# Kernel optimization log

Measured on AMD Instinct MI355X. Metric: run time of the kernel, lower is better.

Reference implementation:

```python
import jax, jax.numpy as jnp
import numpy as np
from jax import lax

MAX_EVENTS = 1024
NHEAD = 8


def _build_events(x, max_events):
    # x: [B, T, C] float in [0,1]. Vectorized run-length encoding.
    B, T, C = x.shape
    xb = (x > 0.5).astype(jnp.int32)
    # run start flags: t=0 is always a start; else value changed vs previous step
    is_start = jnp.concatenate([jnp.ones((B, 1, C), dtype=bool), xb[:, 1:, :] != xb[:, :-1, :]], axis=1)  # [B,T,C]
    t_idx = jnp.arange(T)[None, :, None]  # [1,T,1]
    # next run-start index after t (T if none): suffix-min of start positions
    arr = jnp.where(is_start, t_idx, T)
    suff = lax.cummin(arr, axis=1, reverse=True)
    next_start = jnp.concatenate([suff[:, 1:, :], jnp.full((B, 1, C), T, dtype=suff.dtype)], axis=1)
    duration = next_start - t_idx  # valid at start positions: next change - start
    comp = jnp.arange(C)[None, None, :]
    BIG = jnp.float32(2 * T)
    # sort key identical to torch code: start + component/(C+1); non-starts pushed to the end
    key = jnp.where(is_start, t_idx.astype(jnp.float32) + comp.astype(jnp.float32) / (C + 1.0), BIG)
    keyf = key.reshape(B, T * C)
    order = jnp.argsort(keyf, axis=1)[:, :max_events]  # [B,E] keep earliest events (keys are unique)
    g = lambda a: jnp.take_along_axis(jnp.broadcast_to(a, (B, T, C)).reshape(B, T * C), order, axis=1)
    comp_e = g(comp)
    state_e = g(xb)
    start_e = g(t_idx)
    dur_e = g(duration)
    key_e = jnp.take_along_axis(keyf, order, axis=1)
    mask = (key_e < BIG).astype(x.dtype)  # [B,E]
    onehot = jax.nn.one_hot(comp_e, C, dtype=x.dtype)
    max_start = float(max(1, T - 1))
    rows = jnp.concatenate([
        onehot,
        state_e[..., None].astype(x.dtype),
        start_e[..., None].astype(x.dtype) / max_start,
        dur_e[..., None].astype(x.dtype) / T,
    ], axis=-1)  # [B,E,C+3]
    return rows * mask[..., None], mask


def _ln(z, g, b):
    m = z.mean(-1, keepdims=True)
    v = ((z - m) ** 2).mean(-1, keepdims=True)
    return (z - m) * lax.rsqrt(v + 1e-5) * g + b


def _transformer(h, mask, wq, wk, wv, wo, ln1_g, ln1_b, w1, b1, w2, b2, ln2_g, ln2_b, lnf_g, lnf_b):
    # pre-LN encoder with key-side padding mask; masked mean pooling at the end
    B, E, D = h.shape
    L = wq.shape[0]
    dh = D // NHEAD
    neg = jnp.float32(-1e9)
    kmask = mask[:, None, None, :] > 0  # [B,1,1,E]
    for l in range(L):
        z = _ln(h, ln1_g[l], ln1_b[l])
        q = (z @ wq[l]).reshape(B, E, NHEAD, dh)
        k = (z @ wk[l]).reshape(B, E, NHEAD, dh)
        v = (z @ wv[l]).reshape(B, E, NHEAD, dh)
        s = jnp.einsum('bqhd,bkhd->bhqk', q, k) / jnp.sqrt(jnp.float32(dh))
        s = jnp.where(kmask, s, neg)
        a = jax.nn.softmax(s, axis=-1)
        o = jnp.einsum('bhqk,bkhd->bqhd', a, v).reshape(B, E, D)
        h = h + o @ wo[l]
        z = _ln(h, ln2_g[l], ln2_b[l])
        h = h + (jax.nn.gelu(z @ w1[l] + b1[l]) @ w2[l] + b2[l])
    h = _ln(h, lnf_g, lnf_b)
    denom = jnp.maximum(mask.sum(1, keepdims=True), 1.0)
    return (h * mask[..., None]).sum(1) / denom  # [B,D]


def setup_inputs() -> dict:
    B, T, C = 8, 4096, 8
    D, F, L = 512, 2048, 4
    key = jax.random.key(0)
    ks = jax.random.split(key, 12)
    s = 0.02
    mk = lambda k, shape: jax.random.normal(k, shape, jnp.float32) * s
    return {
        'x': jax.random.uniform(ks[0], (B, T, C), jnp.float32),
        'proj_w': mk(ks[1], (C + 3, D)), 'proj_b': jnp.zeros((D,), jnp.float32),
        'wq': mk(ks[2], (L, D, D)), 'wk': mk(ks[3], (L, D, D)),
        'wv': mk(ks[4], (L, D, D)), 'wo': mk(ks[5], (L, D, D)),
        'ln1_g': jnp.ones((L, D), jnp.float32), 'ln1_b': jnp.zeros((L, D), jnp.float32),
        'w1': mk(ks[6], (L, D, F)), 'b1': jnp.zeros((L, F), jnp.float32),
        'w2': mk(ks[7], (L, F, D)), 'b2': jnp.zeros((L, D), jnp.float32),
        'ln2_g': jnp.ones((L, D), jnp.float32), 'ln2_b': jnp.zeros((L, D), jnp.float32),
        'lnf_g': jnp.ones((D,), jnp.float32), 'lnf_b': jnp.zeros((D,), jnp.float32),
    }


def reference(x, proj_w, proj_b, wq, wk, wv, wo, ln1_g, ln1_b, w1, b1, w2, b2, ln2_g, ln2_b, lnf_g, lnf_b):
    rows, mask = _build_events(x, MAX_EVENTS)
    h = rows @ proj_w + proj_b
    return _transformer(h, mask, wq, wk, wv, wo, ln1_g, ln1_b, w1, b1, w2, b2, ln2_g, ln2_b, lnf_g, lnf_b)
```

## Files before the change

kernel.cpp:

```cpp
#include <hip/hip_runtime.h>
#include <cstdint>
#include <cstddef>


typedef __attribute__((ext_vector_type(8))) short short8;
typedef __attribute__((ext_vector_type(4))) float f32x4;

#define DEVINL __device__ __forceinline__

DEVINL short f2bf(float f) {
  union { float f; unsigned u; } v; v.f = f;
  unsigned u = v.u + 0x7fffu + ((v.u >> 16) & 1u);
  return (short)(u >> 16);
}

DEVINL unsigned bfpack(float lo, float hi) {
  union { float f; unsigned u; } a, b; a.f = lo; b.f = hi;
  return (a.u >> 16) | (b.u & 0xFFFF0000u);
}

DEVINL void gld_lds16(const void* g, void* l) {
  __builtin_amdgcn_global_load_lds(
      (const __attribute__((address_space(1))) void*)g,
      (__attribute__((address_space(3))) void*)l, 16, 0, 0);
}

static constexpr int Bq = 8, T = 4096, C = 8, E = 1024, D = 512, F = 2048;
static constexpr int NL = 4, NH = 8, DH = 64, M = Bq * E;
static constexpr float QSCALE = 0.18033688011112042f;

static constexpr size_t OFF_H    = 0;
static constexpr size_t OFF_Z    = OFF_H    + (size_t)16*1024*1024;
static constexpr size_t OFF_QKV  = OFF_Z    + (size_t)8*1024*1024;
static constexpr size_t OFF_ATT  = OFF_QKV  + (size_t)24*1024*1024;
static constexpr size_t OFF_U    = OFF_ATT  + (size_t)8*1024*1024;
static constexpr size_t OFF_WQKV = OFF_U    + (size_t)32*1024*1024;
static constexpr size_t OFF_WO   = OFF_WQKV + (size_t)6*1024*1024;
static constexpr size_t OFF_W1   = OFF_WO   + (size_t)2*1024*1024;
static constexpr size_t OFF_W2   = OFF_W1   + (size_t)8*1024*1024;
static constexpr size_t OFF_EV   = OFF_W2   + (size_t)8*1024*1024;
static constexpr size_t OFF_NEV  = OFF_EV   + (size_t)131072;
static constexpr size_t OFF_XW   = OFF_NEV  + (size_t)256;

__global__ void tconv_all_kernel(const float* __restrict__ wq, const float* __restrict__ wk,
                                 const float* __restrict__ wv, const float* __restrict__ wo,
                                 const float* __restrict__ w1, const float* __restrict__ w2,
                                 short* __restrict__ wqkv_t, short* __restrict__ wo_t,
                                 short* __restrict__ w1_t, short* __restrict__ w2_t) {
  int bid = blockIdx.x;
  const float* src; short* dst; int N, K, tile;
  if (bid < 4096) {
    int which = bid >> 10, r = bid & 1023, l = r >> 8;
    tile = r & 255; N = 512; K = 512;
    switch (which) {
      case 0:  src = wq + (size_t)l*262144; dst = wqkv_t + (size_t)l*786432;          break;
      case 1:  src = wk + (size_t)l*262144; dst = wqkv_t + (size_t)l*786432 + 262144; break;
      case 2:  src = wv + (size_t)l*262144; dst = wqkv_t + (size_t)l*786432 + 524288; break;
      default: src = wo + (size_t)l*262144; dst = wo_t   + (size_t)l*262144;          break;
    }
  } else if (bid < 8192) {
    int r = bid - 4096, l = r >> 10; tile = r & 1023;
    N = 2048; K = 512;
    src = w1 + (size_t)l*1048576; dst = w1_t + (size_t)l*1048576;
  } else {
    int r = bid - 8192, l = r >> 10; tile = r & 1023;
    N = 512; K = 2048;
    src = w2 + (size_t)l*1048576; dst = w2_t + (size_t)l*1048576;
  }
  int tiles_n = N >> 5;
  int n0 = (tile % tiles_n) * 32, k0 = (tile / tiles_n) * 32;
  __shared__ float tile_s[32][33];
  int tx = threadIdx.x, ty = threadIdx.y;
#pragma unroll
  for (int s = 0; s < 4; ++s)
    tile_s[ty + 8*s][tx] = src[(size_t)(k0 + ty + 8*s) * N + n0 + tx];
  __syncthreads();
#pragma unroll
  for (int s = 0; s < 4; ++s)
    dst[(size_t)(n0 + ty + 8*s) * K + k0 + tx] = f2bf(tile_s[tx][ty + 8*s]);
}

__global__ void xpack_kernel(const float* __restrict__ x, unsigned* __restrict__ xw) {
  __shared__ unsigned char sb[256];
  int idx = blockIdx.x * 256 + threadIdx.x;
  const float* p = x + (size_t)idx * 8;
  f32x4 a = *(const f32x4*)p, b = *(const f32x4*)(p + 4);
  unsigned byte = 0;
#pragma unroll
  for (int j = 0; j < 4; ++j) {
    byte |= (a[j] > 0.5f ? 1u : 0u) << j;
    byte |= (b[j] > 0.5f ? 1u : 0u) << (j + 4);
  }
  sb[threadIdx.x] = (unsigned char)byte;
  __syncthreads();
  if (threadIdx.x < 64)
    xw[blockIdx.x * 64 + threadIdx.x] = *(const unsigned*)(sb + threadIdx.x * 4);
}

__global__ void events_kernel(const unsigned* __restrict__ xw,
                              int4* __restrict__ ev4, int* __restrict__ n_events) {
  int b = blockIdx.x, tid = threadIdx.x;
  int lane = tid & 63, wid = tid >> 6;
  __shared__ int wsum[16];
  const unsigned* xb = xw + b * 1024;
  unsigned word = xb[tid];
  unsigned prevtop = (tid > 0) ? (xb[tid - 1] >> 24) : 0u;
  unsigned flags = word ^ ((word << 8) | prevtop);
  if (tid == 0) flags |= 0xFFu;
  int cnt = __builtin_popcount(flags);

  int v = cnt;
#pragma unroll
  for (int off = 1; off < 64; off <<= 1) {
    int u = __shfl_up(v, off);
    if (lane >= off) v += u;
  }
  if (lane == 63) wsum[wid] = v;
  __syncthreads();
  int base = 0;
  for (int w = 0; w < wid; ++w) base += wsum[w];
  if (tid == 1023) {
    int tot = base + v;
    n_events[b] = tot < E ? tot : E;
  }
  int rank = base + v - cnt;

  unsigned f = flags;
  while (f && rank < E) {
    int bit = __builtin_ctz(f); f &= f - 1;
    int tl = bit >> 3, c = bit & 7;
    int t = tid * 4 + tl;
    int st = (word >> bit) & 1;
    unsigned colm = 0x01010101u << c;
    unsigned above = (bit < 31) ? (flags & colm & (0xFFFFFFFFu << (bit + 1))) : 0u;
    int t2;
    if (above) {
      int nb = __builtin_ctz(above);
      t2 = tid * 4 + ((nb - c) >> 3);
    } else {
      t2 = T;
      for (int w2 = tid + 1; w2 < 1024; ++w2) {
        unsigned nw = xb[w2];
        unsigned fl2 = nw ^ ((nw << 8) | (xb[w2 - 1] >> 24));
        unsigned m2 = fl2 & colm;
        if (m2) { t2 = w2 * 4 + ((__builtin_ctz(m2) - c) >> 3); break; }
      }
    }
    ev4[(b << 10) + rank] = make_int4(c, st, t, t2 - t);
    ++rank;
  }
}

__global__ void embed_kernel(const int4* __restrict__ ev4, const int* __restrict__ nev,
                             const float* __restrict__ pw, const float* __restrict__ pb,
                             float* __restrict__ h) {
  int row = blockIdx.x;
  int b = row >> 10, e = row & 1023;
  int d = threadIdx.x * 4;
  f32x4 acc = *(const f32x4*)(pb + d);
  if (e < nev[b]) {
    int4 e4 = ev4[row];
    float st = (float)e4.y;
    float sn = (float)e4.z * (1.f / 4095.f);
    float dn = (float)e4.w * (1.f / 4096.f);
    acc += *(const f32x4*)(pw + e4.x * D + d);
    acc += st * *(const f32x4*)(pw + 8*D + d);
    acc += sn * *(const f32x4*)(pw + 9*D + d);
    acc += dn * *(const f32x4*)(pw + 10*D + d);
  }
  *(f32x4*)(h + (size_t)row * D + d) = acc;
}

template<int OUTF>
__global__ void ln_kernel(const float* __restrict__ hp, const float* __restrict__ g,
                          const float* __restrict__ bb, void* __restrict__ out) {
  int row = blockIdx.x * 4 + (threadIdx.x >> 6);
  int lane = threadIdx.x & 63;
  int c0 = lane * 8;
  const float* hr = hp + (size_t)row * D;
  f32x4 a = *(const f32x4*)(hr + c0);
  f32x4 c = *(const f32x4*)(hr + c0 + 4);
  float s1 = a[0]+a[1]+a[2]+a[3] + c[0]+c[1]+c[2]+c[3];
  float s2 = a[0]*a[0]+a[1]*a[1]+a[2]*a[2]+a[3]*a[3]
           + c[0]*c[0]+c[1]*c[1]+c[2]*c[2]+c[3]*c[3];
#pragma unroll
  for (int off = 1; off < 64; off <<= 1) {
    s1 += __shfl_xor(s1, off);
    s2 += __shfl_xor(s2, off);
  }
  float mean = s1 * (1.f / 512.f);
  float var  = s2 * (1.f / 512.f) - mean * mean;
  float rstd = rsqrtf(var + 1e-5f);
  f32x4 g0 = *(const f32x4*)(g + c0),  g1 = *(const f32x4*)(g + c0 + 4);
  f32x4 b0 = *(const f32x4*)(bb + c0), b1 = *(const f32x4*)(bb + c0 + 4);
  f32x4 o0 = (a - mean) * rstd * g0 + b0;
  f32x4 o1 = (c - mean) * rstd * g1 + b1;
  if constexpr (OUTF == 0) {
    short8 o;
#pragma unroll
    for (int j = 0; j < 4; ++j) { o[j] = f2bf(o0[j]); o[4 + j] = f2bf(o1[j]); }
    *(short8*)((short*)out + (size_t)row * D + c0) = o;
  } else {
    float* op = (float*)out + (size_t)row * D + c0;
    *(f32x4*)op = o0;
    *(f32x4*)(op + 4) = o1;
  }
}

__global__ void vtrans_kernel(const short* __restrict__ qkv, short* __restrict__ vt) {
  __shared__ short st[64 * 72];
  int et = blockIdx.x, h = blockIdx.y, b = blockIdx.z;
  int tid = threadIdx.x;
  int r8 = tid >> 3, c8 = (tid & 7) * 8;
#pragma unroll
  for (int p = 0; p < 2; ++p) {
    int e = r8 + p * 32;
    short8 v = *(const short8*)(qkv + (size_t)(b*1024 + et*64 + e) * 1536 + 1024 + h*64 + c8);
#pragma unroll
    for (int j = 0; j < 8; ++j) st[(c8 + j) * 72 + e] = v[j];
  }
  __syncthreads();
#pragma unroll
  for (int p = 0; p < 2; ++p) {
    int dd = r8 + p * 32;
    short8 o = *(const short8*)(st + dd * 72 + c8);
    *(short8*)(vt + ((size_t)((b*8 + h) * 64 + dd)) * 1024 + et * 64 + c8) = o;
  }
}

template<int MODE>
__global__ __launch_bounds__(256, 4)
void gemm_kernel(const short* __restrict__ A, const short* __restrict__ Bt,
                 const float* __restrict__ bias, short* __restrict__ O1,
                 int N, int K) {
  __shared__ short a_s[2][128 * 32];
  __shared__ short b_s[2][128 * 32];
  const int tid = threadIdx.x;
  const int wid = tid >> 6, lane = tid & 63;
  const int quad = lane >> 4, l16 = lane & 15;
  const int m0 = blockIdx.y * 128, n0 = blockIdx.x * 128;
  const int wrow = wid >> 1, wcol = wid & 1;
  const int nk = K >> 5;

  const int row0 = tid >> 2, kc0 = tid & 3;
  const int row1 = (tid + 256) >> 2;
  const int ks0 = (kc0 ^ ((row0 >> 1) & 3)) * 8;
  const int ks1 = (kc0 ^ ((row1 >> 1) & 3)) * 8;
  const int ldsoff0 = tid * 8 - lane * 8;
  const int ldsoff1 = (tid + 256) * 8 - lane * 8;

  auto stage = [&](int kt, int buf) {
    int k0 = kt * 32;
    gld_lds16(A  + (size_t)(m0 + row0) * K + k0 + ks0, a_s[buf] + ldsoff0);
    gld_lds16(A  + (size_t)(m0 + row1) * K + k0 + ks1, a_s[buf] + ldsoff1);
    gld_lds16(Bt + (size_t)(n0 + row0) * K + k0 + ks0, b_s[buf] + ldsoff0);
    gld_lds16(Bt + (size_t)(n0 + row1) * K + k0 + ks1, b_s[buf] + ldsoff1);
  };

  f32x4 acc[4][4] = {};

  stage(0, 0);
  asm volatile("s_waitcnt vmcnt(0)" ::: "memory");
  __syncthreads();

  for (int kt = 0; kt < nk; ++kt) {
    const int cur = kt & 1;
    const bool more = (kt + 1) < nk;
    if (more) stage(kt + 1, cur ^ 1);

    short8 af[4], bf[4];
#pragma unroll
    for (int mi = 0; mi < 4; ++mi) {
      int row = wrow*64 + mi*16 + l16;
      int sw = quad ^ ((row >> 1) & 3);
      af[mi] = *(const short8*)(a_s[cur] + row * 32 + sw * 8);
    }
#pragma unroll
    for (int ni = 0; ni < 4; ++ni) {
      int row = wcol*64 + ni*16 + l16;
      int sw = quad ^ ((row >> 1) & 3);
      bf[ni] = *(const short8*)(b_s[cur] + row * 32 + sw * 8);
    }
#pragma unroll
    for (int mi = 0; mi < 4; ++mi)
#pragma unroll
      for (int ni = 0; ni < 4; ++ni)
        acc[mi][ni] = __builtin_amdgcn_mfma_f32_16x16x32_bf16(af[mi], bf[ni], acc[mi][ni], 0, 0, 0);

    if (more) {
      asm volatile("s_waitcnt vmcnt(0)" ::: "memory");
      __syncthreads();
    }
  }

  const int mb = m0 + wrow * 64, nb = n0 + wcol * 64;
#pragma unroll
  for (int mi = 0; mi < 4; ++mi) {
#pragma unroll
    for (int ni = 0; ni < 4; ++ni) {
      int nn = nb + ni * 16 + l16;
#pragma unroll
      for (int r = 0; r < 4; ++r) {
        int mm = mb + mi * 16 + quad * 4 + r;
        float cv = acc[mi][ni][r];
        if constexpr (MODE == 0) {
          float ov = (nn < 512) ? cv * QSCALE : cv;
          union { float f; unsigned u; } vv; vv.f = ov;
          O1[(size_t)mm * N + nn] = (short)(vv.u >> 16);
        } else {
          float xv = cv + bias[nn];
          float x3 = xv * (1.f + 0.044715f * xv * xv);
          float ez = __builtin_amdgcn_exp2f(-2.3022082299f * x3);
          float gv = xv * __builtin_amdgcn_rcpf(1.f + ez);
          union { float f; unsigned u; } vv; vv.f = gv;
          O1[(size_t)mm * N + nn] = (short)(vv.u >> 16);
        }
      }
    }
  }
}

__global__ __launch_bounds__(256, 4)
void gemm64_kernel(const short* __restrict__ A, const short* __restrict__ Bt,
                   const float* __restrict__ bias, float* __restrict__ Cr,
                   int N, int K) {
  __shared__ short a_s[2][64 * 32];
  __shared__ short b_s[2][128 * 32];
  const int tid = threadIdx.x;
  const int wid = tid >> 6, lane = tid & 63;
  const int quad = lane >> 4, l16 = lane & 15;
  const int m0 = blockIdx.y * 64, n0 = blockIdx.x * 128;
  const int nk = K >> 5;

  const int row0 = tid >> 2, kc0 = tid & 3;
  const int row1 = (tid + 256) >> 2;
  const int ksA  = (kc0 ^ (((row0 & 63) >> 1) & 3)) * 8;
  const int ks0  = (kc0 ^ ((row0 >> 1) & 3)) * 8;
  const int ks1  = (kc0 ^ ((row1 >> 1) & 3)) * 8;
  const int ldsoff0 = tid * 8 - lane * 8;
  const int ldsoff1 = (tid + 256) * 8 - lane * 8;

  auto stage = [&](int kt, int buf) {
    int k0 = kt * 32;
    gld_lds16(A  + (size_t)(m0 + row0) * K + k0 + ksA, a_s[buf] + ldsoff0);
    gld_lds16(Bt + (size_t)(n0 + row0) * K + k0 + ks0, b_s[buf] + ldsoff0);
    gld_lds16(Bt + (size_t)(n0 + row1) * K + k0 + ks1, b_s[buf] + ldsoff1);
  };

  f32x4 acc[4][2] = {};

  stage(0, 0);
  asm volatile("s_waitcnt vmcnt(0)" ::: "memory");
  __syncthreads();

  for (int kt = 0; kt < nk; ++kt) {
    const int cur = kt & 1;
    const bool more = (kt + 1) < nk;
    if (more) stage(kt + 1, cur ^ 1);

    short8 af[4], bf[2];
#pragma unroll
    for (int mi = 0; mi < 4; ++mi) {
      int row = mi*16 + l16;
      int sw = quad ^ ((row >> 1) & 3);
      af[mi] = *(const short8*)(a_s[cur] + row * 32 + sw * 8);
    }
#pragma unroll
    for (int ni = 0; ni < 2; ++ni) {
      int row = wid*32 + ni*16 + l16;
      int sw = quad ^ ((row >> 1) & 3);
      bf[ni] = *(const short8*)(b_s[cur] + row * 32 + sw * 8);
    }
#pragma unroll
    for (int mi = 0; mi < 4; ++mi)
#pragma unroll
      for (int ni = 0; ni < 2; ++ni)
        acc[mi][ni] = __builtin_amdgcn_mfma_f32_16x16x32_bf16(af[mi], bf[ni], acc[mi][ni], 0, 0, 0);

    if (more) {
      asm volatile("s_waitcnt vmcnt(0)" ::: "memory");
      __syncthreads();
    }
  }

#pragma unroll
  for (int mi = 0; mi < 4; ++mi) {
#pragma unroll
    for (int ni = 0; ni < 2; ++ni) {
      int nn = n0 + wid*32 + ni * 16 + l16;
#pragma unroll
      for (int r = 0; r < 4; ++r) {
        int mm = m0 + mi * 16 + quad * 4 + r;
        float add = acc[mi][ni][r] + (bias ? bias[nn] : 0.f);
        Cr[(size_t)mm * N + nn] += add;
      }
    }
  }
}

__global__ __launch_bounds__(256, 4)
void attn_kernel(const short* __restrict__ qkv, const short* __restrict__ vt,
                 short* __restrict__ att, const int* __restrict__ n_events) {
  __shared__ short q_s[64 * 64];
  __shared__ short k_s[64 * 64];
  __shared__ short vt_s[64 * 64];
  __shared__ short p_s[64 * 68];
  const int tid = threadIdx.x, wid = tid >> 6, lane = tid & 63;
  const int quad = lane >> 4, l16 = lane & 15;
  const int qt = blockIdx.x, h = blockIdx.y, b = blockIdx.z;
  const int ne = n_events[b];
  const int qbase = b * E + qt * 64;

#pragma unroll
  for (int r = 0; r < 2; ++r) {
    int row = wid * 16 + r * 8 + (lane >> 3);
    int sz = lane & 7, dc = sz ^ (row & 7);
    gld_lds16(qkv + (size_t)(qbase + row) * 1536 + h * 64 + dc * 8,
              q_s + (wid * 16 + r * 8) * 64);
  }
  asm volatile("s_waitcnt vmcnt(0)" ::: "memory");

  short8 qf[2];
#pragma unroll
  for (int ks = 0; ks < 2; ++ks) {
    int row = wid * 16 + l16;
    int dc = (ks * 4 + quad) ^ (row & 7);
    qf[ks] = *(const short8*)(q_s + row * 64 + dc * 8);
  }

  f32x4 accO[4] = {};
  float rs = 0.f;

  for (int kt = 0; kt < 16; ++kt) {
    __syncthreads();
#pragma unroll
    for (int r = 0; r < 2; ++r) {
      int i = (r*4 + wid) * 64 + lane;
      int row = i >> 3, sz = i & 7, dc = sz ^ (row & 7);
      gld_lds16(qkv + (size_t)(b * E + kt * 64 + row) * 1536 + 512 + h * 64 + dc * 8,
                k_s + (r*4 + wid) * 512);
      gld_lds16(vt + (size_t)((b * 8 + h) * 64 + row) * 1024 + kt * 64 + dc * 8,
                vt_s + (r*4 + wid) * 512);
    }
    asm volatile("s_waitcnt vmcnt(0)" ::: "memory");
    __syncthreads();

    f32x4 accS[4] = {};
#pragma unroll
    for (int ni = 0; ni < 4; ++ni) {
#pragma unroll
      for (int ks = 0; ks < 2; ++ks) {
        int row = ni * 16 + l16;
        int dc = (ks * 4 + quad) ^ (row & 7);
        short8 kf = *(const short8*)(k_s + row * 64 + dc * 8);
        accS[ni] = __builtin_amdgcn_mfma_f32_16x16x32_bf16(kf, qf[ks], accS[ni], 0, 0, 0);
      }
    }

    bool full = (kt * 64 + 64) <= ne;
#pragma unroll
    for (int ni = 0; ni < 4; ++ni) {
      float p[4];
#pragma unroll
      for (int r = 0; r < 4; ++r) {
        bool masked = !full && (kt * 64 + ni * 16 + quad * 4 + r) >= ne;
        p[r] = masked ? 0.f : __builtin_amdgcn_exp2f(accS[ni][r]);
        rs += p[r];
      }
      unsigned w0 = bfpack(p[0], p[1]), w1 = bfpack(p[2], p[3]);
      int2 pk; pk.x = (int)w0; pk.y = (int)w1;
      *(int2*)(p_s + (wid * 16 + l16) * 68 + ni * 16 + quad * 4) = pk;
    }

    short8 ap[2];
#pragma unroll
    for (int ks = 0; ks < 2; ++ks)
      ap[ks] = *(const short8*)(p_s + (wid * 16 + l16) * 68 + ks * 32 + quad * 8);
#pragma unroll
    for (int di = 0; di < 4; ++di) {
#pragma unroll
      for (int ks = 0; ks < 2; ++ks) {
        int dd = di * 16 + l16;
        int dc = (ks * 4 + quad) ^ (dd & 7);
        short8 bv = *(const short8*)(vt_s + dd * 64 + dc * 8);
        accO[di] = __builtin_amdgcn_mfma_f32_16x16x32_bf16(ap[ks], bv, accO[di], 0, 0, 0);
      }
    }
  }

  rs += __shfl_xor(rs, 16);
  rs += __shfl_xor(rs, 32);
#pragma unroll
  for (int r = 0; r < 4; ++r) {
    float dv = __shfl(rs, quad * 4 + r);
    float linv = 1.f / (dv > 0.f ? dv : 1.f);
    int mm = qbase + wid * 16 + quad * 4 + r;
#pragma unroll
    for (int di = 0; di < 4; ++di)
      att[(size_t)mm * D + h * 64 + di * 16 + l16] = f2bf(accO[di][r] * linv);
  }
}

__global__ void pool_kernel(const float* __restrict__ tmp, const int* __restrict__ nev,
                            float* __restrict__ out) {
  __shared__ float red[512];
  int b = blockIdx.x >> 6, ch = blockIdx.x & 63;
  int n = nev[b];
  float inv = 1.f / (float)(n > 0 ? n : 1);
  int tid = threadIdx.x;
  int col = (tid & 127) * 4;
  int r0 = ch * 16 + (tid >> 7);
  f32x4 s = {0.f, 0.f, 0.f, 0.f};
#pragma unroll
  for (int i = 0; i < 8; ++i) {
    int e = r0 + i * 2;
    if (e < n) s += *(const f32x4*)(tmp + ((size_t)(b * E + e)) * D + col);
  }
  if (tid >= 128) *(f32x4*)(red + (tid - 128) * 4) = s;
  __syncthreads();
  if (tid < 128) {
    s += *(const f32x4*)(red + tid * 4);
#pragma unroll
    for (int j = 0; j < 4; ++j) atomicAdd(&out[b * D + col + j], s[j] * inv);
  }
}

extern "C" void kernel_launch(void* const* d_in, const int* in_sizes, int n_in,
                              void* d_out, int out_size, void* d_ws, size_t ws_size,
                              hipStream_t stream) {
  (void)in_sizes; (void)n_in; (void)ws_size;
  const float* x      = (const float*)d_in[0];
  const float* proj_w = (const float*)d_in[1];
  const float* proj_b = (const float*)d_in[2];
  const float* wq     = (const float*)d_in[3];
  const float* wk     = (const float*)d_in[4];
  const float* wv     = (const float*)d_in[5];
  const float* wo     = (const float*)d_in[6];
  const float* ln1_g  = (const float*)d_in[7];
  const float* ln1_b  = (const float*)d_in[8];
  const float* w1     = (const float*)d_in[9];
  const float* b1     = (const float*)d_in[10];
  const float* w2     = (const float*)d_in[11];
  const float* b2     = (const float*)d_in[12];
  const float* ln2_g  = (const float*)d_in[13];
  const float* ln2_b  = (const float*)d_in[14];
  const float* lnf_g  = (const float*)d_in[15];
  const float* lnf_b  = (const float*)d_in[16];

  char* ws = (char*)d_ws;
  float* h      = (float*)(ws + OFF_H);
  short* z      = (short*)(ws + OFF_Z);
  short* qkv    = (short*)(ws + OFF_QKV);
  short* att    = (short*)(ws + OFF_ATT);
  short* u      = (short*)(ws + OFF_U);
  short* vt     = (short*)(ws + OFF_U);
  float* tmp    = (float*)(ws + OFF_U);
  short* wqkv_t = (short*)(ws + OFF_WQKV);
  short* wo_t   = (short*)(ws + OFF_WO);
  short* w1_t   = (short*)(ws + OFF_W1);
  short* w2_t   = (short*)(ws + OFF_W2);
  int4*  ev4    = (int4*)(ws + OFF_EV);
  int*   n_ev   = (int*)(ws + OFF_NEV);
  unsigned* xw  = (unsigned*)(ws + OFF_XW);

  tconv_all_kernel<<<12288, dim3(32,8), 0, stream>>>(wq, wk, wv, wo, w1, w2,
                                                     wqkv_t, wo_t, w1_t, w2_t);
  xpack_kernel<<<128, 256, 0, stream>>>(x, xw);
  events_kernel<<<8, 1024, 0, stream>>>(xw, ev4, n_ev);
  embed_kernel<<<M, 128, 0, stream>>>(ev4, n_ev, proj_w, proj_b, h);

  for (int l = 0; l < NL; ++l) {
    ln_kernel<0><<<2048, 256, 0, stream>>>(h, ln1_g + l*D, ln1_b + l*D, z);
    gemm_kernel<0><<<dim3(12,64), 256, 0, stream>>>(z, wqkv_t + (size_t)l*786432, nullptr, qkv, 1536, 512);
    vtrans_kernel<<<dim3(16,8,8), 256, 0, stream>>>(qkv, vt);
    attn_kernel<<<dim3(16,8,8), 256, 0, stream>>>(qkv, vt, att, n_ev);
    gemm64_kernel<<<dim3(4,128), 256, 0, stream>>>(att, wo_t + (size_t)l*262144, nullptr, h, 512, 512);
    ln_kernel<0><<<2048, 256, 0, stream>>>(h, ln2_g + l*D, ln2_b + l*D, z);
    gemm_kernel<1><<<dim3(16,64), 256, 0, stream>>>(z, w1_t + (size_t)l*1048576, b1 + l*F, u, 2048, 512);
    gemm64_kernel<<<dim3(4,128), 256, 0, stream>>>(u, w2_t + (size_t)l*1048576, b2 + l*D, h, 512, 2048);
  }

  ln_kernel<1><<<2048, 256, 0, stream>>>(h, lnf_g, lnf_b, tmp);
  hipMemsetAsync(d_out, 0, (size_t)out_size * sizeof(float), stream);
  pool_kernel<<<512, 256, 0, stream>>>(tmp, n_ev, (float*)d_out);
}
```

Baseline: 797.6 us.

## Remap GEMM/attention blocks to XCDs and double K-tile in gemm64

Turns the 2D/3D launch grids of the GEMM and attention kernels into 1D grids. Block ids are remapped so that blocks sharing the same A rows (or the same batch/head) land on the same XCD, which should improve L2 reuse on the chiplet-based MI355X. Separately, the gemm64 kernel now uses a 64-wide K tile with an 8-way XOR swizzle. This halves the number of k-iterations and barriers, at the cost of more LDS and a lower occupancy bound (launch_bounds 4→3).

```diff
diff --git a/kernel.cpp b/kernel.cpp
--- a/kernel.cpp
+++ b/kernel.cpp
@@ -228,7 +228,7 @@
   }
 }
 
-template<int MODE>
+template<int MODE, int NX>
 __global__ __launch_bounds__(256, 4)
 void gemm_kernel(const short* __restrict__ A, const short* __restrict__ Bt,
                  const float* __restrict__ bias, short* __restrict__ O1,
@@ -238,7 +238,9 @@
   const int tid = threadIdx.x;
   const int wid = tid >> 6, lane = tid & 63;
   const int quad = lane >> 4, l16 = lane & 15;
-  const int m0 = blockIdx.y * 128, n0 = blockIdx.x * 128;
+  const int bid = blockIdx.x;
+  const int xcd = bid & 7, q = bid >> 3;
+  const int m0 = ((q / NX) * 8 + xcd) * 128, n0 = (q % NX) * 128;
   const int wrow = wid >> 1, wcol = wid & 1;
   const int nk = K >> 5;
 
@@ -320,31 +322,36 @@
   }
 }
 
-__global__ __launch_bounds__(256, 4)
+__global__ __launch_bounds__(256, 3)
 void gemm64_kernel(const short* __restrict__ A, const short* __restrict__ Bt,
                    const float* __restrict__ bias, float* __restrict__ Cr,
                    int N, int K) {
-  __shared__ short a_s[2][64 * 32];
-  __shared__ short b_s[2][128 * 32];
+  __shared__ short a_s[2][64 * 64];
+  __shared__ short b_s[2][128 * 64];
   const int tid = threadIdx.x;
   const int wid = tid >> 6, lane = tid & 63;
   const int quad = lane >> 4, l16 = lane & 15;
-  const int m0 = blockIdx.y * 64, n0 = blockIdx.x * 128;
-  const int nk = K >> 5;
-
-  const int row0 = tid >> 2, kc0 = tid & 3;
-  const int row1 = (tid + 256) >> 2;
-  const int ksA  = (kc0 ^ (((row0 & 63) >> 1) & 3)) * 8;
-  const int ks0  = (kc0 ^ ((row0 >> 1) & 3)) * 8;
-  const int ks1  = (kc0 ^ ((row1 >> 1) & 3)) * 8;
-  const int ldsoff0 = tid * 8 - lane * 8;
-  const int ldsoff1 = (tid + 256) * 8 - lane * 8;
+  const int bid = blockIdx.x;
+  const int xcd = bid & 7, q = bid >> 3;
+  const int m0 = ((q >> 2) * 8 + xcd) * 64, n0 = (q & 3) * 128;
+  const int nk = K >> 6;
 
   auto stage = [&](int kt, int buf) {
-    int k0 = kt * 32;
-    gld_lds16(A  + (size_t)(m0 + row0) * K + k0 + ksA, a_s[buf] + ldsoff0);
-    gld_lds16(Bt + (size_t)(n0 + row0) * K + k0 + ks0, b_s[buf] + ldsoff0);
-    gld_lds16(Bt + (size_t)(n0 + row1) * K + k0 + ks1, b_s[buf] + ldsoff1);
+    int k0 = kt * 64;
+#pragma unroll
+    for (int j = 0; j < 2; ++j) {
+      int i = tid + j * 256;
+      int row = i >> 3, kc = i & 7;
+      int ks = (kc ^ (row & 7)) * 8;
+      gld_lds16(A + (size_t)(m0 + row) * K + k0 + ks, a_s[buf] + i * 8 - lane * 8);
+    }
+#pragma unroll
+    for (int j = 0; j < 4; ++j) {
+      int i = tid + j * 256;
+      int row = i >> 3, kc = i & 7;
+      int ks = (kc ^ (row & 7)) * 8;
+      gld_lds16(Bt + (size_t)(n0 + row) * K + k0 + ks, b_s[buf] + i * 8 - lane * 8);
+    }
   };
 
   f32x4 acc[4][2] = {};
@@ -358,24 +365,32 @@
     const bool more = (kt + 1) < nk;
     if (more) stage(kt + 1, cur ^ 1);
 
-    short8 af[4], bf[2];
+    short8 af[4][2], bf[2][2];
 #pragma unroll
     for (int mi = 0; mi < 4; ++mi) {
       int row = mi*16 + l16;
-      int sw = quad ^ ((row >> 1) & 3);
-      af[mi] = *(const short8*)(a_s[cur] + row * 32 + sw * 8);
+#pragma unroll
+      for (int ks = 0; ks < 2; ++ks) {
+        int sw = (ks * 4 + quad) ^ (row & 7);
+        af[mi][ks] = *(const short8*)(a_s[cur] + row * 64 + sw * 8);
+      }
     }
 #pragma unroll
     for (int ni = 0; ni < 2; ++ni) {
       int row = wid*32 + ni*16 + l16;
-      int sw = quad ^ ((row >> 1) & 3);
-      bf[ni] = *(const short8*)(b_s[cur] + row * 32 + sw * 8);
+#pragma unroll
+      for (int ks = 0; ks < 2; ++ks) {
+        int sw = (ks * 4 + quad) ^ (row & 7);
+        bf[ni][ks] = *(const short8*)(b_s[cur] + row * 64 + sw * 8);
+      }
     }
 #pragma unroll
     for (int mi = 0; mi < 4; ++mi)
 #pragma unroll
       for (int ni = 0; ni < 2; ++ni)
-        acc[mi][ni] = __builtin_amdgcn_mfma_f32_16x16x32_bf16(af[mi], bf[ni], acc[mi][ni], 0, 0, 0);
+#pragma unroll
+        for (int ks = 0; ks < 2; ++ks)
+          acc[mi][ni] = __builtin_amdgcn_mfma_f32_16x16x32_bf16(af[mi][ks], bf[ni][ks], acc[mi][ni], 0, 0, 0);
 
     if (more) {
       asm volatile("s_waitcnt vmcnt(0)" ::: "memory");
@@ -407,7 +422,11 @@
   __shared__ short p_s[64 * 68];
   const int tid = threadIdx.x, wid = tid >> 6, lane = tid & 63;
   const int quad = lane >> 4, l16 = lane & 15;
-  const int qt = blockIdx.x, h = blockIdx.y, b = blockIdx.z;
+  const int bid = blockIdx.x;
+  const int xcd = bid & 7, qq = bid >> 3;
+  const int qt = qq & 15;
+  const int bh = (qq >> 4) * 8 + xcd;
+  const int b = bh >> 3, h = bh & 7;
   const int ne = n_events[b];
   const int qbase = b * E + qt * 64;
 
@@ -571,13 +590,13 @@
 
   for (int l = 0; l < NL; ++l) {
     ln_kernel<0><<<2048, 256, 0, stream>>>(h, ln1_g + l*D, ln1_b + l*D, z);
-    gemm_kernel<0><<<dim3(12,64), 256, 0, stream>>>(z, wqkv_t + (size_t)l*786432, nullptr, qkv, 1536, 512);
+    gemm_kernel<0,12><<<768, 256, 0, stream>>>(z, wqkv_t + (size_t)l*786432, nullptr, qkv, 1536, 512);
     vtrans_kernel<<<dim3(16,8,8), 256, 0, stream>>>(qkv, vt);
-    attn_kernel<<<dim3(16,8,8), 256, 0, stream>>>(qkv, vt, att, n_ev);
-    gemm64_kernel<<<dim3(4,128), 256, 0, stream>>>(att, wo_t + (size_t)l*262144, nullptr, h, 512, 512);
+    attn_kernel<<<1024, 256, 0, stream>>>(qkv, vt, att, n_ev);
+    gemm64_kernel<<<512, 256, 0, stream>>>(att, wo_t + (size_t)l*262144, nullptr, h, 512, 512);
     ln_kernel<0><<<2048, 256, 0, stream>>>(h, ln2_g + l*D, ln2_b + l*D, z);
-    gemm_kernel<1><<<dim3(16,64), 256, 0, stream>>>(z, w1_t + (size_t)l*1048576, b1 + l*F, u, 2048, 512);
-    gemm64_kernel<<<dim3(4,128), 256, 0, stream>>>(u, w2_t + (size_t)l*1048576, b2 + l*D, h, 512, 2048);
+    gemm_kernel<1,16><<<1024, 256, 0, stream>>>(z, w1_t + (size_t)l*1048576, b1 + l*F, u, 2048, 512);
+    gemm64_kernel<<<512, 256, 0, stream>>>(u, w2_t + (size_t)l*1048576, b2 + l*D, h, 512, 2048);
   }
 
   ln_kernel<1><<<2048, 256, 0, stream>>>(h, lnf_g, lnf_b, tmp);
```

New measurement: 734.2 us. -8.0%, faster.
